# Kernel tuning notes

Hardware: AMD Instinct MI355X
Metric: run time of the kernel (lower is better)

The kernel has to match this reference:

```python
import jax, jax.numpy as jnp
import numpy as np

EPS = 1e-5

def _ln_channels(x, w, b):
    # LayerNorm over channel dim of BCHW (original permutes to BHWC, LN on C)
    mu = jnp.mean(x, axis=1, keepdims=True)
    var = jnp.mean(jnp.square(x - mu), axis=1, keepdims=True)
    xn = (x - mu) * jax.lax.rsqrt(var + EPS)
    return xn * w[None, :, None, None] + b[None, :, None, None]

def _conv1x1(x, w, b):
    # 1x1 conv == per-pixel GEMM over channels
    return jnp.einsum('oc,bchw->bohw', w, x) + b[None, :, None, None]

def setup_inputs() -> dict:
    key = jax.random.key(0)
    ks = jax.random.split(key, 5)
    B, C, H, W = 8, 256, 160, 160
    hid = 2 * C
    s = lambda fan_in: 1.0 / np.sqrt(fan_in)
    return {
        'x': jax.random.normal(ks[0], (B, C, H, W), jnp.float32),
        'ln1_w': jnp.ones((C,), jnp.float32),
        'ln1_b': jnp.zeros((C,), jnp.float32),
        'qkv_w': jax.random.normal(ks[1], (3 * C, C), jnp.float32) * s(C),
        'qkv_b': jnp.zeros((3 * C,), jnp.float32),
        'proj_w': jax.random.normal(ks[2], (C, C), jnp.float32) * s(C),
        'proj_b': jnp.zeros((C,), jnp.float32),
        'ln2_w': jnp.ones((C,), jnp.float32),
        'ln2_b': jnp.zeros((C,), jnp.float32),
        'w1': jax.random.normal(ks[3], (hid, C), jnp.float32) * s(C),
        'b1': jnp.zeros((hid,), jnp.float32),
        'w2': jax.random.normal(ks[4], (C, hid), jnp.float32) * s(hid),
        'b2': jnp.zeros((C,), jnp.float32),
    }

def reference(x, ln1_w, ln1_b, qkv_w, qkv_b, proj_w, proj_b, ln2_w, ln2_b, w1, b1, w2, b2):
    B, C, H, W = x.shape
    # --- attention branch ---
    xn = _ln_channels(x, ln1_w, ln1_b)
    qkv = _conv1x1(xn, qkv_w, qkv_b)            # (B, 3C, H, W)
    q, k, v = jnp.split(qkv, 3, axis=1)
    q = q.reshape(B, C, H * W)                   # (B, C, N)
    k = k.reshape(B, C, H * W)
    v = v.reshape(B, C, H * W)
    # channel attention: (B, C, C) scores, softmax over last (channel) axis
    scores = jnp.einsum('bcn,bdn->bcd', q, k) / jnp.sqrt(jnp.asarray(C, x.dtype))
    attn = jax.nn.softmax(scores, axis=-1)
    out = jnp.einsum('bcd,bdn->bcn', attn, v).reshape(B, C, H, W)
    x = x + _conv1x1(out, proj_w, proj_b)
    # --- conv FFN branch ---
    yn = _ln_channels(x, ln2_w, ln2_b)
    h = jax.nn.gelu(_conv1x1(yn, w1, b1), approximate=False)
    x = x + _conv1x1(h, w2, b2)
    return x
```

## Files before the change

### kernel.cpp

```cpp
#include <hip/hip_runtime.h>

#define Bc   8
#define Cc   256
#define NP   25600
#define HIDc 512
#define EPSc 1e-5f

typedef __bf16 bf16_t;
typedef __bf16 bf16x8_t __attribute__((ext_vector_type(8)));
typedef float  f32x4_t  __attribute__((ext_vector_type(4)));

__device__ __forceinline__ unsigned short f2bf_u(float f) {
  bf16_t t = (bf16_t)f;
  return __builtin_bit_cast(unsigned short, t);
}

__device__ __forceinline__ float gelu_f(float x) {
  float x3 = x * x * x;
  float y = 0.7978845608028654f * (x + 0.044715f * x3);
  float e = __expf(2.0f * y);
  float t = 1.0f - 2.0f * __builtin_amdgcn_rcpf(1.0f + e);
  return 0.5f * x * (1.0f + t);
}

__device__ __forceinline__ void glds16(const void* g, void* l) {
  __builtin_amdgcn_global_load_lds(
      (const __attribute__((address_space(1))) unsigned int*)g,
      (__attribute__((address_space(3))) unsigned int*)l,
      16, 0, 0);
}


__global__ __launch_bounds__(256) void k_ln1(const float* __restrict__ x,
                                             const float* __restrict__ gamma,
                                             const float* __restrict__ beta,
                                             bf16_t* __restrict__ cf,
                                             bf16_t* __restrict__ cl) {
  int bb = blockIdx.y;
  int n0 = blockIdx.x * 64;
  int t = threadIdx.x;
  int w = t >> 6, l = t & 63;
  __shared__ bf16_t X[256 * 64];
  __shared__ float R2[4][64][2];
  const float* xb = x + (size_t)bb * Cc * NP;
  float s1 = 0.f, s2 = 0.f;
#pragma unroll 8
  for (int co = 0; co < 64; ++co) {
    int c = w * 64 + co;
    float v = xb[(size_t)c * NP + n0 + l];
    s1 += v; s2 += v * v;
    X[c * 64 + l] = (bf16_t)v;
  }
  R2[w][l][0] = s1; R2[w][l][1] = s2;
  __syncthreads();
  int px = t & 63, gq = t >> 6;
  float ts1 = R2[0][px][0] + R2[1][px][0] + R2[2][px][0] + R2[3][px][0];
  float ts2 = R2[0][px][1] + R2[1][px][1] + R2[2][px][1] + R2[3][px][1];
  float mu = ts1 * (1.0f / Cc);
  float rstd = rsqrtf(ts2 * (1.0f / Cc) - mu * mu + EPSc);
  bf16_t* cfp = cf + (size_t)bb * Cc * NP;
  bf16_t* clp = cl + (size_t)bb * NP * Cc + (size_t)(n0 + px) * Cc;
#pragma unroll
  for (int chunk = 0; chunk < 8; ++chunk) {
    union { uint4 u; unsigned short us[8]; } pk;
#pragma unroll
    for (int e = 0; e < 8; ++e) {
      int c = gq * 64 + chunk * 8 + e;
      float xv = (float)X[c * 64 + px];
      float v = (xv - mu) * rstd * gamma[c] + beta[c];
      unsigned short bu = f2bf_u(v);
      pk.us[e] = bu;
      cfp[(size_t)c * NP + n0 + px] = __builtin_bit_cast(bf16_t, bu);
    }
    *(uint4*)(clp + gq * 64 + chunk * 8) = pk.u;
  }
}

__global__ __launch_bounds__(256) void k_gram_mfma(const bf16_t* __restrict__ xn,
                                                   float* __restrict__ G) {
  int b = blockIdx.z;
  int ti = blockIdx.y >> 1, tj = blockIdx.y & 1;
  int t = threadIdx.x;
  int l = t & 63, qq = l >> 4, rr = l & 15;
  int wv = t >> 6;
  int wm = (wv >> 1) * 64, wn = (wv & 1) * 64;
  int row8 = l >> 3, sl = l & 7;
  int s = (sl - row8) & 7;
  __shared__ bf16_t At[128 * 64];
  __shared__ bf16_t Bt[128 * 64];
  const bf16_t* xb = xn + (size_t)b * Cc * NP;
  const bf16_t* gA = xb + (size_t)(ti * 128 + wv * 32 + row8) * NP + s * 8;
  const bf16_t* gB = xb + (size_t)(tj * 128 + wv * 32 + row8) * NP + s * 8;
  f32x4_t acc[4][4] = {};
  int k0 = blockIdx.x * 1600;
  int kend = k0 + 1600;
  for (; k0 < kend; k0 += 64) {
#pragma unroll
    for (int i = 0; i < 4; ++i) {
      glds16(gA + (size_t)(i * 8) * NP + k0, At + (wv * 32 + i * 8) * 64);
      glds16(gB + (size_t)(i * 8) * NP + k0, Bt + (wv * 32 + i * 8) * 64);
    }
    __syncthreads();
#pragma unroll
    for (int h = 0; h < 2; ++h) {
      bf16x8_t af[4], bff[4];
#pragma unroll
      for (int mi = 0; mi < 4; ++mi) {
        int row = wm + mi * 16 + rr;
        int g = (h * 4 + qq + (row & 7)) & 7;
        af[mi] = *(const bf16x8_t*)&At[row * 64 + g * 8];
      }
#pragma unroll
      for (int nj = 0; nj < 4; ++nj) {
        int row = wn + nj * 16 + rr;
        int g = (h * 4 + qq + (row & 7)) & 7;
        bff[nj] = *(const bf16x8_t*)&Bt[row * 64 + g * 8];
      }
#pragma unroll
      for (int mi = 0; mi < 4; ++mi)
#pragma unroll
        for (int nj = 0; nj < 4; ++nj)
          acc[mi][nj] = __builtin_amdgcn_mfma_f32_16x16x32_bf16(af[mi], bff[nj], acc[mi][nj], 0, 0, 0);
    }
    __syncthreads();
  }
  float* Gb = G + (size_t)b * Cc * Cc;
#pragma unroll
  for (int mi = 0; mi < 4; ++mi)
#pragma unroll
    for (int nj = 0; nj < 4; ++nj) {
      int col = tj * 128 + wn + nj * 16 + rr;
#pragma unroll
      for (int reg = 0; reg < 4; ++reg) {
        int rowc = ti * 128 + wm + mi * 16 + qq * 4 + reg;
        atomicAdd(&Gb[(size_t)rowc * Cc + col], acc[mi][nj][reg]);
      }
    }
}

__global__ __launch_bounds__(256) void k_small_T(const float* __restrict__ G,
                                                 const float* __restrict__ qkv_w,
                                                 float* __restrict__ T) {
  int b = blockIdx.y, e = blockIdx.x, d = threadIdx.x;
  __shared__ float gs[Cc];
  gs[d] = G[((size_t)b * Cc + e) * Cc + d];
  __syncthreads();
  const float* wk = qkv_w + (size_t)(Cc + d) * Cc;
  float acc = 0.f;
  for (int f = 0; f < Cc; ++f) acc += gs[f] * wk[f];
  T[((size_t)b * Cc + e) * Cc + d] = acc;
}
__global__ __launch_bounds__(256) void k_small_SP(const float* __restrict__ T,
                                                  const float* __restrict__ qkv_w,
                                                  const float* __restrict__ qkv_b,
                                                  float* __restrict__ P,
                                                  float* __restrict__ pv) {
  int b = blockIdx.y, c0 = blockIdx.x, d = threadIdx.x;
  __shared__ float wq[Cc];
  wq[d] = qkv_w[(size_t)c0 * Cc + d];
  __syncthreads();
  const float* Tb = T + (size_t)b * Cc * Cc;
  float acc = 0.f;
  for (int e = 0; e < Cc; ++e) acc += wq[e] * Tb[(size_t)e * Cc + d];
  float v = acc * 0.0625f;
  __shared__ float red[256];
  red[d] = v; __syncthreads();
  for (int sd = 128; sd > 0; sd >>= 1) { if (d < sd) red[d] = fmaxf(red[d], red[d + sd]); __syncthreads(); }
  float m = red[0]; __syncthreads();
  float e1 = expf(v - m);
  red[d] = e1; __syncthreads();
  for (int sd = 128; sd > 0; sd >>= 1) { if (d < sd) red[d] += red[d + sd]; __syncthreads(); }
  float inv = 1.0f / red[0]; __syncthreads();
  float p = e1 * inv;
  P[((size_t)b * Cc + c0) * Cc + d] = p;
  red[d] = p * qkv_b[2 * Cc + d]; __syncthreads();
  for (int sd = 128; sd > 0; sd >>= 1) { if (d < sd) red[d] += red[d + sd]; __syncthreads(); }
  if (d == 0) pv[(size_t)b * Cc + c0] = red[0];
}
__global__ __launch_bounds__(256) void k_small_U(const float* __restrict__ P,
                                                 const float* __restrict__ qkv_w,
                                                 float* __restrict__ U) {
  int b = blockIdx.y, c = blockIdx.x, e = threadIdx.x;
  __shared__ float pr[Cc];
  pr[e] = P[((size_t)b * Cc + c) * Cc + e];
  __syncthreads();
  float acc = 0.f;
  for (int d = 0; d < Cc; ++d) acc += pr[d] * qkv_w[(size_t)(2 * Cc + d) * Cc + e];
  U[((size_t)b * Cc + c) * Cc + e] = acc;
}
__global__ __launch_bounds__(256) void k_small_A2(const float* __restrict__ U,
                                                  const float* __restrict__ proj_w,
                                                  const float* __restrict__ proj_b,
                                                  const float* __restrict__ pv,
                                                  bf16_t* __restrict__ A2b_out,
                                                  float* __restrict__ a2b) {
  int b = blockIdx.y, o = blockIdx.x, e = threadIdx.x;
  __shared__ float wr[Cc];
  wr[e] = proj_w[(size_t)o * Cc + e];
  __syncthreads();
  const float* Ub = U + (size_t)b * Cc * Cc;
  float acc = 0.f;
  for (int c = 0; c < Cc; ++c) acc += wr[c] * Ub[(size_t)c * Cc + e];
  A2b_out[((size_t)b * Cc + o) * Cc + e] = (bf16_t)acc;
  __shared__ float red[256];
  red[e] = wr[e] * pv[(size_t)b * Cc + e];
  __syncthreads();
  for (int sd = 128; sd > 0; sd >>= 1) { if (e < sd) red[e] += red[e + sd]; __syncthreads(); }
  if (e == 0) a2b[(size_t)b * Cc + o] = red[0] + proj_b[o];
}

__global__ __launch_bounds__(256) void k_f2b(const float* __restrict__ s,
                                             bf16_t* __restrict__ d, int n) {
  int i = (blockIdx.x * 256 + threadIdx.x) * 4;
  if (i >= n) return;
  float4 v = *(const float4*)(s + i);
  ushort4 pk;
  pk.x = f2bf_u(v.x); pk.y = f2bf_u(v.y); pk.z = f2bf_u(v.z); pk.w = f2bf_u(v.w);
  *(ushort4*)(d + i) = pk;
}

__global__ __launch_bounds__(512) void k_apply_ln(
    const bf16_t* __restrict__ A2b, const bf16_t* __restrict__ xn,
    const float* __restrict__ a2b, const float* __restrict__ xres,
    const float* __restrict__ g2, const float* __restrict__ b2,
    float* __restrict__ out, bf16_t* __restrict__ yn) {
  int b = blockIdx.y;
  int n0 = blockIdx.x * 128;
  int t = threadIdx.x;
  int w = t >> 6, l = t & 63;
  int qq = l >> 4, rr = l & 15;
  int wmW = w >> 1, wnW = w & 1;
  int row8 = l >> 3, sl = l & 7;
  int s = (sl - row8) & 7;

  __shared__ char SM[53248];
  bf16_t* At = (bf16_t*)SM;
  bf16_t* Bt = (bf16_t*)(SM + 32768);
  bf16_t* Tt = (bf16_t*)SM;
  float*  Red = (float*)(SM + 49152);

  const bf16_t* Ab = A2b + (size_t)b * Cc * Cc;
  const bf16_t* xb = xn + (size_t)b * (size_t)NP * Cc;
  const bf16_t* gA = Ab + (size_t)(w * 32 + row8) * Cc + s * 8;
  const bf16_t* gB = xb + (size_t)(n0 + w * 16 + row8) * Cc + s * 8;
  f32x4_t acc[4][4] = {};
  for (int k0 = 0; k0 < Cc; k0 += 64) {
#pragma unroll
    for (int i = 0; i < 4; ++i)
      glds16(gA + (size_t)(i * 8) * Cc + k0, At + (w * 32 + i * 8) * 64);
#pragma unroll
    for (int i = 0; i < 2; ++i)
      glds16(gB + (size_t)(i * 8) * Cc + k0, Bt + (w * 16 + i * 8) * 64);
    __syncthreads();
#pragma unroll
    for (int h = 0; h < 2; ++h) {
      bf16x8_t af[4], bff[4];
#pragma unroll
      for (int mi = 0; mi < 4; ++mi) {
        int row = wmW * 64 + mi * 16 + rr;
        int g = (h * 4 + qq + (row & 7)) & 7;
        af[mi] = *(const bf16x8_t*)&At[row * 64 + g * 8];
      }
#pragma unroll
      for (int nj = 0; nj < 4; ++nj) {
        int row = wnW * 64 + nj * 16 + rr;
        int g = (h * 4 + qq + (row & 7)) & 7;
        bff[nj] = *(const bf16x8_t*)&Bt[row * 64 + g * 8];
      }
#pragma unroll
      for (int mi = 0; mi < 4; ++mi)
#pragma unroll
        for (int nj = 0; nj < 4; ++nj)
          acc[mi][nj] = __builtin_amdgcn_mfma_f32_16x16x32_bf16(af[mi], bff[nj], acc[mi][nj], 0, 0, 0);
    }
    __syncthreads();
  }

  const float* ab = a2b + (size_t)b * Cc;
  const float* rp = xres + (size_t)b * Cc * NP;
  float* op = out + (size_t)b * Cc * NP;
  float s1[4] = {}, s2[4] = {};
#pragma unroll
  for (int mi = 0; mi < 4; ++mi) {
    int ch0 = wmW * 64 + mi * 16 + qq * 4;
    float4 abv = *(const float4*)(ab + ch0);
#pragma unroll
    for (int nj = 0; nj < 4; ++nj) {
      int px = n0 + wnW * 64 + nj * 16 + rr;
#pragma unroll
      for (int reg = 0; reg < 4; ++reg) {
        float v = acc[mi][nj][reg] + ((const float*)&abv)[reg] + rp[(size_t)(ch0 + reg) * NP + px];
        acc[mi][nj][reg] = v;
        s1[nj] += v; s2[nj] += v * v;
      }
    }
  }
#pragma unroll
  for (int nj = 0; nj < 4; ++nj) {
    s1[nj] += __shfl_xor(s1[nj], 16); s2[nj] += __shfl_xor(s2[nj], 16);
    s1[nj] += __shfl_xor(s1[nj], 32); s2[nj] += __shfl_xor(s2[nj], 32);
  }
  if (qq == 0) {
#pragma unroll
    for (int nj = 0; nj < 4; ++nj) {
      int colb = wnW * 64 + nj * 16 + rr;
      Red[(wmW * 128 + colb) * 2 + 0] = s1[nj];
      Red[(wmW * 128 + colb) * 2 + 1] = s2[nj];
    }
  }
  __syncthreads();
  float mu[4], rstd[4];
#pragma unroll
  for (int nj = 0; nj < 4; ++nj) {
    int colb = wnW * 64 + nj * 16 + rr;
    float t1 = 0.f, t2 = 0.f;
#pragma unroll
    for (int mw = 0; mw < 4; ++mw) {
      t1 += Red[(mw * 128 + colb) * 2 + 0];
      t2 += Red[(mw * 128 + colb) * 2 + 1];
    }
    mu[nj] = t1 * (1.0f / Cc);
    rstd[nj] = rsqrtf(t2 * (1.0f / Cc) - mu[nj] * mu[nj] + EPSc);
  }
#pragma unroll
  for (int mi = 0; mi < 4; ++mi) {
    int ch0 = wmW * 64 + mi * 16 + qq * 4;
#pragma unroll
    for (int nj = 0; nj < 4; ++nj) {
      int px = n0 + wnW * 64 + nj * 16 + rr;
#pragma unroll
      for (int reg = 0; reg < 4; ++reg)
        op[(size_t)(ch0 + reg) * NP + px] = acc[mi][nj][reg];
    }
  }
  bf16_t* yb = yn + (size_t)b * (size_t)NP * Cc;
#pragma unroll
  for (int hh = 0; hh < 2; ++hh) {
    __syncthreads();
    if ((wmW >> 1) == hh) {
#pragma unroll
      for (int mi = 0; mi < 4; ++mi) {
        int ch0 = wmW * 64 + mi * 16 + qq * 4;
        int chloc = (wmW & 1) * 64 + mi * 16 + qq * 4;
        float4 gv = *(const float4*)(g2 + ch0);
        float4 bv = *(const float4*)(b2 + ch0);
#pragma unroll
        for (int nj = 0; nj < 4; ++nj) {
          int colb = wnW * 64 + nj * 16 + rr;
          ushort4 pk;
#pragma unroll
          for (int reg = 0; reg < 4; ++reg) {
            float yv = (acc[mi][nj][reg] - mu[nj]) * rstd[nj] * ((const float*)&gv)[reg] + ((const float*)&bv)[reg];
            ((unsigned short*)&pk)[reg] = f2bf_u(yv);
          }
          *(ushort4*)&Tt[colb * 136 + chloc] = pk;
        }
      }
    }
    __syncthreads();
#pragma unroll
    for (int i = 0; i < 4; ++i) {
      int idx = i * 512 + t;
      int row = idx >> 4, ch16 = idx & 15;
      uint4 v4 = *(const uint4*)&Tt[row * 136 + ch16 * 8];
      *(uint4*)&yb[(size_t)(n0 + row) * Cc + hh * 128 + ch16 * 8] = v4;
    }
  }
}

__global__ __launch_bounds__(512) void k_ffn(
    const bf16_t* __restrict__ w1b,
    const bf16_t* __restrict__ w2b,
    const float* __restrict__ b1,
    const float* __restrict__ b2,
    const bf16_t* __restrict__ yn,
    float* __restrict__ out) {
  int b = blockIdx.y;
  int n0 = blockIdx.x * 128;
  int t = threadIdx.x;
  int w = t >> 6, l = t & 63;
  int qq = l >> 4, rr = l & 15;
  int row8 = l >> 3, sl = l & 7;
  int s = (sl - row8) & 7;
  int aM = (w >> 2) * 64;
  int aN = (w & 3) * 32;
  int bM = (w >> 1) * 64;
  int bN = (w & 1) * 64;

  __shared__ bf16_t St[2][16384];
  __shared__ bf16_t H[128 * 128];
  __shared__ float b1s[HIDc];
  __shared__ float b2s[Cc];

  b1s[t] = b1[t];
  if (t < Cc) b2s[t] = b2[t];

  const bf16_t* ynb = yn + (size_t)b * (size_t)NP * Cc;

  auto stageA = [&](int slot, int hc, int ks) {
#pragma unroll
    for (int i = 0; i < 2; ++i) {
      const bf16_t* gw = w1b + (size_t)(hc * 128 + w * 16 + i * 8 + row8) * Cc + ks * 64 + s * 8;
      glds16(gw, &St[slot][(w * 16 + i * 8) * 64]);
    }
#pragma unroll
    for (int i = 0; i < 2; ++i) {
      const bf16_t* gy = ynb + (size_t)(n0 + w * 16 + i * 8 + row8) * Cc + ks * 64 + s * 8;
      glds16(gy, &St[slot][8192 + (w * 16 + i * 8) * 64]);
    }
  };
  auto stageW2 = [&](int slot, int hc, int tt) {
#pragma unroll
    for (int i = 0; i < 4; ++i) {
      const bf16_t* gw = w2b + (size_t)(w * 32 + i * 8 + row8) * HIDc + hc * 128 + tt * 64 + s * 8;
      glds16(gw, &St[slot][(w * 32 + i * 8) * 64]);
    }
  };
  auto computeA = [&](int slot, f32x4_t (&accA)[4][2]) {
#pragma unroll
    for (int h = 0; h < 2; ++h) {
      bf16x8_t af[4], bf_[2];
#pragma unroll
      for (int mi = 0; mi < 4; ++mi) {
        int row = aM + mi * 16 + rr;
        int g = (h * 4 + qq + (row & 7)) & 7;
        af[mi] = *(const bf16x8_t*)&St[slot][row * 64 + g * 8];
      }
#pragma unroll
      for (int nj = 0; nj < 2; ++nj) {
        int row = aN + nj * 16 + rr;
        int g = (h * 4 + qq + (row & 7)) & 7;
        bf_[nj] = *(const bf16x8_t*)&St[slot][8192 + row * 64 + g * 8];
      }
#pragma unroll
      for (int mi = 0; mi < 4; ++mi)
#pragma unroll
        for (int nj = 0; nj < 2; ++nj)
          accA[mi][nj] = __builtin_amdgcn_mfma_f32_16x16x32_bf16(af[mi], bf_[nj], accA[mi][nj], 0, 0, 0);
    }
  };
  auto writeH = [&](int hc, f32x4_t (&accA)[4][2]) {
#pragma unroll
    for (int mi = 0; mi < 4; ++mi) {
      int hid_l = aM + mi * 16 + qq * 4;
      float4 b1v = *(const float4*)&b1s[hc * 128 + hid_l];
#pragma unroll
      for (int nj = 0; nj < 2; ++nj) {
        int px = aN + nj * 16 + rr;
        union { ushort4 pk; uint2 u2; } u;
#pragma unroll
        for (int reg = 0; reg < 4; ++reg) {
          float v = accA[mi][nj][reg] + ((const float*)&b1v)[reg];
          ((unsigned short*)&u.pk)[reg] = f2bf_u(gelu_f(v));
        }
        int slot8 = hid_l >> 2;
        int sp = (slot8 + 3 * (px & 15)) & 31;
        *(uint2*)&H[px * 128 + sp * 4] = u.u2;
      }
    }
  };

  f32x4_t accB[4][4] = {};
  stageA(0, 0, 0);
  int cur = 0;
  for (int hc = 0; hc < 4; ++hc) {
    f32x4_t accA[4][2] = {};
    for (int ks = 0; ks < 4; ++ks) {
      if (ks < 3) stageA(cur ^ 1, hc, ks + 1);
      else        stageW2(cur ^ 1, hc, 0);
      asm volatile("s_waitcnt vmcnt(4)" ::: "memory");
      __builtin_amdgcn_s_barrier();
      __builtin_amdgcn_sched_barrier(0);
      computeA(cur, accA);
      if (ks == 3) {
        writeH(hc, accA);
        asm volatile("s_waitcnt lgkmcnt(0)" ::: "memory");
      }
      __builtin_amdgcn_sched_barrier(0);
      __builtin_amdgcn_s_barrier();
      cur ^= 1;
    }
    for (int tt = 0; tt < 2; ++tt) {
      bool last = (hc == 3) && (tt == 1);
      if (!last) {
        if (tt == 0) stageW2(cur ^ 1, hc, 1);
        else         stageA(cur ^ 1, hc + 1, 0);
        asm volatile("s_waitcnt vmcnt(4)" ::: "memory");
      } else {
        asm volatile("s_waitcnt vmcnt(0)" ::: "memory");
      }
      __builtin_amdgcn_s_barrier();
      __builtin_amdgcn_sched_barrier(0);
#pragma unroll
      for (int h = 0; h < 2; ++h) {
        bf16x8_t af[4], bf_[4];
#pragma unroll
        for (int mi = 0; mi < 4; ++mi) {
          int row = bM + mi * 16 + rr;
          int g = (h * 4 + qq + (row & 7)) & 7;
          af[mi] = *(const bf16x8_t*)&St[cur][row * 64 + g * 8];
        }
#pragma unroll
        for (int nj = 0; nj < 4; ++nj) {
          int px = bN + nj * 16 + rr;
          int s0 = tt * 16 + h * 8 + qq * 2;
          int sp0 = (s0 + 3 * (px & 15)) & 31;
          int sp1 = (s0 + 1 + 3 * (px & 15)) & 31;
          union { bf16x8_t v; uint2 u[2]; } tmp;
          tmp.u[0] = *(const uint2*)&H[px * 128 + sp0 * 4];
          tmp.u[1] = *(const uint2*)&H[px * 128 + sp1 * 4];
          bf_[nj] = tmp.v;
        }
#pragma unroll
        for (int mi = 0; mi < 4; ++mi)
#pragma unroll
          for (int nj = 0; nj < 4; ++nj)
            accB[mi][nj] = __builtin_amdgcn_mfma_f32_16x16x32_bf16(af[mi], bf_[nj], accB[mi][nj], 0, 0, 0);
      }
      __builtin_amdgcn_sched_barrier(0);
      __builtin_amdgcn_s_barrier();
      cur ^= 1;
    }
  }
  float* ob = out + (size_t)b * Cc * NP;
#pragma unroll
  for (int mi = 0; mi < 4; ++mi) {
    int ch = bM + mi * 16 + qq * 4;
    float4 b2v = *(const float4*)&b2s[ch];
#pragma unroll
    for (int nj = 0; nj < 4; ++nj) {
      int px = n0 + bN + nj * 16 + rr;
#pragma unroll
      for (int reg = 0; reg < 4; ++reg) {
        float* p = ob + (size_t)(ch + reg) * NP + px;
        *p = accB[mi][nj][reg] + ((const float*)&b2v)[reg] + *p;
      }
    }
  }
}

extern "C" void kernel_launch(void* const* d_in, const int* in_sizes, int n_in,
                              void* d_out, int out_size, void* d_ws, size_t ws_size,
                              hipStream_t stream) {
  const float* x     = (const float*)d_in[0];
  const float* ln1w  = (const float*)d_in[1];
  const float* ln1b  = (const float*)d_in[2];
  const float* qkvw  = (const float*)d_in[3];
  const float* qkvb  = (const float*)d_in[4];
  const float* projw = (const float*)d_in[5];
  const float* projb = (const float*)d_in[6];
  const float* ln2w  = (const float*)d_in[7];
  const float* ln2b  = (const float*)d_in[8];
  const float* w1    = (const float*)d_in[9];
  const float* b1    = (const float*)d_in[10];
  const float* w2    = (const float*)d_in[11];
  const float* b2    = (const float*)d_in[12];
  float* out = (float*)d_out;

  char* ws = (char*)d_ws;
  const size_t XNCL_B = (size_t)Bc * NP * Cc * 2;
  const size_t CF_B   = (size_t)Bc * NP * Cc * 2;
  bf16_t* xn_cl = (bf16_t*)ws;
  bf16_t* xn_cf = (bf16_t*)(ws + XNCL_B);
  char* sm = ws + XNCL_B + CF_B;
  float* G   = (float*)sm;
  float* S   = G + (size_t)Bc * Cc * Cc;
  float* T   = S + (size_t)Bc * Cc * Cc;
  float* pv  = T + (size_t)Bc * Cc * Cc;
  float* a2b = pv + 2048;
  bf16_t* A2b = (bf16_t*)(a2b + 2048);
  bf16_t* w1b = A2b + (size_t)Bc * Cc * Cc;
  bf16_t* w2b = w1b + (size_t)HIDc * Cc;
  float* U = T;

  k_f2b<<<dim3(HIDc * Cc / 1024), 256, 0, stream>>>(w1, w1b, HIDc * Cc);
  k_f2b<<<dim3(Cc * HIDc / 1024), 256, 0, stream>>>(w2, w2b, Cc * HIDc);

  k_ln1<<<dim3(NP / 64, Bc), 256, 0, stream>>>(x, ln1w, ln1b, xn_cf, xn_cl);
  hipMemsetAsync(G, 0, (size_t)Bc * Cc * Cc * 4, stream);
  k_gram_mfma<<<dim3(16, 4, Bc), 256, 0, stream>>>(xn_cf, G);
  k_small_T<<<dim3(Cc, Bc), 256, 0, stream>>>(G, qkvw, T);
  k_small_SP<<<dim3(Cc, Bc), 256, 0, stream>>>(T, qkvw, qkvb, S, pv);
  k_small_U<<<dim3(Cc, Bc), 256, 0, stream>>>(S, qkvw, U);
  k_small_A2<<<dim3(Cc, Bc), 256, 0, stream>>>(U, projw, projb, pv, A2b, a2b);
  k_apply_ln<<<dim3(NP / 128, Bc), 512, 0, stream>>>(
      A2b, xn_cl, a2b, x, ln2w, ln2b, out, xn_cl);

  k_ffn<<<dim3(NP / 128, Bc), 512, 0, stream>>>(w1b, w2b, b1, b2, xn_cl, out);

  (void)in_sizes; (void)n_in; (void)out_size; (void)ws_size;
}
```

Before: 771.1 us.

## Shrink FFN block to 64 pixels, single-buffer LDS, drop software pipelining

The FFN kernel now uses 256 threads covering 64 pixels per block instead of 512 threads covering 128, with one LDS staging buffer and a half-size hidden tile, and it no longer overlaps global-to-LDS loads with MFMA compute. Each step loads, syncs, computes, then syncs again. The smaller LDS footprint is meant to let more blocks fit per CU so occupancy hides latency in place of explicit double buffering. In exchange, each block reloads the full W1/W2 weights for half as many pixels, doubling weight traffic per pixel, and the load-compute overlap inside a block is lost.

```diff
diff --git a/kernel.cpp b/kernel.cpp
--- a/kernel.cpp
+++ b/kernel.cpp
@@ -368,7 +368,7 @@
   }
 }
 
-__global__ __launch_bounds__(512) void k_ffn(
+__global__ __launch_bounds__(256) void k_ffn(
     const bf16_t* __restrict__ w1b,
     const bf16_t* __restrict__ w2b,
     const float* __restrict__ b1,
@@ -376,70 +376,62 @@
     const bf16_t* __restrict__ yn,
     float* __restrict__ out) {
   int b = blockIdx.y;
-  int n0 = blockIdx.x * 128;
+  int n0 = blockIdx.x * 64;
   int t = threadIdx.x;
-  int w = t >> 6, l = t & 63;
+  int wv = t >> 6, l = t & 63;
   int qq = l >> 4, rr = l & 15;
   int row8 = l >> 3, sl = l & 7;
   int s = (sl - row8) & 7;
-  int aM = (w >> 2) * 64;
-  int aN = (w & 3) * 32;
-  int bM = (w >> 1) * 64;
-  int bN = (w & 1) * 64;
-
-  __shared__ bf16_t St[2][16384];
-  __shared__ bf16_t H[128 * 128];
+  int aM = (wv >> 1) * 64;
+  int aN = (wv & 1) * 32;
+  int bM = wv * 64;
+
+  __shared__ bf16_t St[16384];
+  __shared__ bf16_t H[64 * 128];
   __shared__ float b1s[HIDc];
   __shared__ float b2s[Cc];
 
-  b1s[t] = b1[t];
-  if (t < Cc) b2s[t] = b2[t];
+  b1s[t] = b1[t]; b1s[t + 256] = b1[t + 256];
+  b2s[t] = b2[t];
 
   const bf16_t* ynb = yn + (size_t)b * (size_t)NP * Cc;
-
-  auto stageA = [&](int slot, int hc, int ks) {
-#pragma unroll
-    for (int i = 0; i < 2; ++i) {
-      const bf16_t* gw = w1b + (size_t)(hc * 128 + w * 16 + i * 8 + row8) * Cc + ks * 64 + s * 8;
-      glds16(gw, &St[slot][(w * 16 + i * 8) * 64]);
-    }
-#pragma unroll
-    for (int i = 0; i < 2; ++i) {
-      const bf16_t* gy = ynb + (size_t)(n0 + w * 16 + i * 8 + row8) * Cc + ks * 64 + s * 8;
-      glds16(gy, &St[slot][8192 + (w * 16 + i * 8) * 64]);
-    }
-  };
-  auto stageW2 = [&](int slot, int hc, int tt) {
-#pragma unroll
-    for (int i = 0; i < 4; ++i) {
-      const bf16_t* gw = w2b + (size_t)(w * 32 + i * 8 + row8) * HIDc + hc * 128 + tt * 64 + s * 8;
-      glds16(gw, &St[slot][(w * 32 + i * 8) * 64]);
-    }
-  };
-  auto computeA = [&](int slot, f32x4_t (&accA)[4][2]) {
-#pragma unroll
-    for (int h = 0; h < 2; ++h) {
-      bf16x8_t af[4], bf_[2];
-#pragma unroll
-      for (int mi = 0; mi < 4; ++mi) {
-        int row = aM + mi * 16 + rr;
-        int g = (h * 4 + qq + (row & 7)) & 7;
-        af[mi] = *(const bf16x8_t*)&St[slot][row * 64 + g * 8];
-      }
-#pragma unroll
-      for (int nj = 0; nj < 2; ++nj) {
-        int row = aN + nj * 16 + rr;
-        int g = (h * 4 + qq + (row & 7)) & 7;
-        bf_[nj] = *(const bf16x8_t*)&St[slot][8192 + row * 64 + g * 8];
-      }
-#pragma unroll
-      for (int mi = 0; mi < 4; ++mi)
-#pragma unroll
-        for (int nj = 0; nj < 2; ++nj)
-          accA[mi][nj] = __builtin_amdgcn_mfma_f32_16x16x32_bf16(af[mi], bf_[nj], accA[mi][nj], 0, 0, 0);
-    }
-  };
-  auto writeH = [&](int hc, f32x4_t (&accA)[4][2]) {
+  f32x4_t accB[4][4] = {};
+
+  for (int hc = 0; hc < 4; ++hc) {
+    f32x4_t accA[4][2] = {};
+    for (int ks = 0; ks < 4; ++ks) {
+#pragma unroll
+      for (int i = 0; i < 4; ++i)
+        glds16(w1b + (size_t)(hc * 128 + wv * 32 + i * 8 + row8) * Cc + ks * 64 + s * 8,
+               St + (wv * 32 + i * 8) * 64);
+#pragma unroll
+      for (int i = 0; i < 2; ++i)
+        glds16(ynb + (size_t)(n0 + wv * 16 + i * 8 + row8) * Cc + ks * 64 + s * 8,
+               St + 8192 + (wv * 16 + i * 8) * 64);
+      __syncthreads();
+#pragma unroll
+      for (int h = 0; h < 2; ++h) {
+        bf16x8_t af[4], bf_[2];
+#pragma unroll
+        for (int mi = 0; mi < 4; ++mi) {
+          int row = aM + mi * 16 + rr;
+          int g = (h * 4 + qq + (row & 7)) & 7;
+          af[mi] = *(const bf16x8_t*)&St[row * 64 + g * 8];
+        }
+#pragma unroll
+        for (int nj = 0; nj < 2; ++nj) {
+          int row = aN + nj * 16 + rr;
+          int g = (h * 4 + qq + (row & 7)) & 7;
+          bf_[nj] = *(const bf16x8_t*)&St[8192 + row * 64 + g * 8];
+        }
+#pragma unroll
+        for (int mi = 0; mi < 4; ++mi)
+#pragma unroll
+          for (int nj = 0; nj < 2; ++nj)
+            accA[mi][nj] = __builtin_amdgcn_mfma_f32_16x16x32_bf16(af[mi], bf_[nj], accA[mi][nj], 0, 0, 0);
+      }
+      __syncthreads();
+    }
 #pragma unroll
     for (int mi = 0; mi < 4; ++mi) {
       int hid_l = aM + mi * 16 + qq * 4;
@@ -458,39 +450,13 @@
         *(uint2*)&H[px * 128 + sp * 4] = u.u2;
       }
     }
-  };
-
-  f32x4_t accB[4][4] = {};
-  stageA(0, 0, 0);
-  int cur = 0;
-  for (int hc = 0; hc < 4; ++hc) {
-    f32x4_t accA[4][2] = {};
-    for (int ks = 0; ks < 4; ++ks) {
-      if (ks < 3) stageA(cur ^ 1, hc, ks + 1);
-      else        stageW2(cur ^ 1, hc, 0);
-      asm volatile("s_waitcnt vmcnt(4)" ::: "memory");
-      __builtin_amdgcn_s_barrier();
-      __builtin_amdgcn_sched_barrier(0);
-      computeA(cur, accA);
-      if (ks == 3) {
-        writeH(hc, accA);
-        asm volatile("s_waitcnt lgkmcnt(0)" ::: "memory");
-      }
-      __builtin_amdgcn_sched_barrier(0);
-      __builtin_amdgcn_s_barrier();
-      cur ^= 1;
-    }
+    __syncthreads();
     for (int tt = 0; tt < 2; ++tt) {
-      bool last = (hc == 3) && (tt == 1);
-      if (!last) {
-        if (tt == 0) stageW2(cur ^ 1, hc, 1);
-        else         stageA(cur ^ 1, hc + 1, 0);
-        asm volatile("s_waitcnt vmcnt(4)" ::: "memory");
-      } else {
-        asm volatile("s_waitcnt vmcnt(0)" ::: "memory");
-      }
-      __builtin_amdgcn_s_barrier();
-      __builtin_amdgcn_sched_barrier(0);
+#pragma unroll
+      for (int i = 0; i < 8; ++i)
+        glds16(w2b + (size_t)(wv * 64 + i * 8 + row8) * HIDc + hc * 128 + tt * 64 + s * 8,
+               St + (wv * 64 + i * 8) * 64);
+      __syncthreads();
 #pragma unroll
       for (int h = 0; h < 2; ++h) {
         bf16x8_t af[4], bf_[4];
@@ -498,11 +464,11 @@
         for (int mi = 0; mi < 4; ++mi) {
           int row = bM + mi * 16 + rr;
           int g = (h * 4 + qq + (row & 7)) & 7;
-          af[mi] = *(const bf16x8_t*)&St[cur][row * 64 + g * 8];
+          af[mi] = *(const bf16x8_t*)&St[row * 64 + g * 8];
         }
 #pragma unroll
         for (int nj = 0; nj < 4; ++nj) {
-          int px = bN + nj * 16 + rr;
+          int px = nj * 16 + rr;
           int s0 = tt * 16 + h * 8 + qq * 2;
           int sp0 = (s0 + 3 * (px & 15)) & 31;
           int sp1 = (s0 + 1 + 3 * (px & 15)) & 31;
@@ -517,9 +483,7 @@
           for (int nj = 0; nj < 4; ++nj)
             accB[mi][nj] = __builtin_amdgcn_mfma_f32_16x16x32_bf16(af[mi], bf_[nj], accB[mi][nj], 0, 0, 0);
       }
-      __builtin_amdgcn_sched_barrier(0);
-      __builtin_amdgcn_s_barrier();
-      cur ^= 1;
+      __syncthreads();
     }
   }
   float* ob = out + (size_t)b * Cc * NP;
@@ -529,7 +493,7 @@
     float4 b2v = *(const float4*)&b2s[ch];
 #pragma unroll
     for (int nj = 0; nj < 4; ++nj) {
-      int px = n0 + bN + nj * 16 + rr;
+      int px = n0 + nj * 16 + rr;
 #pragma unroll
       for (int reg = 0; reg < 4; ++reg) {
         float* p = ob + (size_t)(ch + reg) * NP + px;
@@ -586,7 +550,7 @@
   k_apply_ln<<<dim3(NP / 128, Bc), 512, 0, stream>>>(
       A2b, xn_cl, a2b, x, ln2w, ln2b, out, xn_cl);
 
-  k_ffn<<<dim3(NP / 128, Bc), 512, 0, stream>>>(w1b, w2b, b1, b2, xn_cl, out);
+  k_ffn<<<dim3(NP / 64, Bc), 256, 0, stream>>>(w1b, w2b, b1, b2, xn_cl, out);
 
   (void)in_sizes; (void)n_in; (void)out_size; (void)ws_size;
 }
```

Measured after the change: 845.0 us. 1.1x slower.
